# Kernel tuning notes

Measured on AMD Instinct MI355X. Metric: run time of the kernel, lower is better.

Reference implementation:

```python
import jax, jax.numpy as jnp
import numpy as np

INPUT_SIZE = 10000
GROUP_SIZE = 500
STEP = GROUP_SIZE // 2            # 250
OUT_PER_GROUP = 50
GROUPS = 2 * INPUT_SIZE // GROUP_SIZE - 1  # 39


def setup_inputs() -> dict:
    key = jax.random.key(0)
    k1, k2 = jax.random.split(key)
    x = jax.random.uniform(k1, (4096, INPUT_SIZE), dtype=jnp.float32)
    # torch init: uniform_(weight, 0.9, 1.1); weight shape per group is [out, in]
    W = jax.random.uniform(k2, (GROUPS, OUT_PER_GROUP, GROUP_SIZE),
                           dtype=jnp.float32, minval=0.9, maxval=1.1)
    return {"x": x, "W": W}


def reference(x, W):
    # gather overlapping windows: idx[g, k] = g*STEP + k  -> [B, GROUPS, GROUP_SIZE]
    idx = jnp.arange(GROUPS)[:, None] * STEP + jnp.arange(GROUP_SIZE)[None, :]
    xw = x[:, idx]                                   # [B, G, K]
    # per-group linear (no bias): out[b,g,o] = sum_k xw[b,g,k] * W[g,o,k]
    out = jnp.einsum('bgk,gok->bgo', xw, W)          # [B, G, O]
    return jax.nn.relu(out.reshape(x.shape[0], GROUPS * OUT_PER_GROUP))
```

## Files before the change

### kernel.cpp

```cpp
#include <hip/hip_runtime.h>
#include <hip/hip_bf16.h>


constexpr int INPUT  = 10000;
constexpr int GROUPS = 39;
constexpr int GS     = 500;
constexpr int STEP   = 250;
constexpr int OPG    = 50;
constexpr int OUTW   = 1950;
constexpr int KP     = 512;
constexpr int BM     = 32;
constexpr int LDA    = KP + 8;

__device__ __hip_bfloat16 Wb[GROUPS * OPG * KP];

typedef __attribute__((ext_vector_type(8))) short  short8;
typedef __attribute__((ext_vector_type(4))) float  float4v;

__device__ __forceinline__ unsigned bf2pack(float a, float b) {
    union { float f; unsigned u; } x, y; x.f = a; y.f = b;
    unsigned lo = (x.u + 0x7fffu + ((x.u >> 16) & 1u)) >> 16;
    unsigned hi = (y.u + 0x7fffu + ((y.u >> 16) & 1u)) & 0xffff0000u;
    return hi | lo;
}

__global__ void prep_w(const float* __restrict__ W) {
    const int slot = blockIdx.x * 256 + threadIdx.x;
    if (slot >= GROUPS * OPG * (KP / 2)) return;
    const int go = slot / (KP / 2);
    const int k  = (slot - go * (KP / 2)) * 2;
    float2 v = {0.f, 0.f};
    if (k < GS) v = *(const float2*)(W + (size_t)go * GS + k);
    ((unsigned*)Wb)[slot] = bf2pack(v.x, v.y);
}

__global__ __launch_bounds__(256, 4)
void peak_binner_kernel(const float* __restrict__ x,
                        float* __restrict__ out, int batch)
{
    __shared__ __align__(16) short As[BM * LDA];

    const int g    = blockIdx.x;
    const int m0   = blockIdx.y * BM;
    const int tid  = threadIdx.x;
    const int lane = tid & 63;
    const int wave = tid >> 6;
    const int fm   = lane & 15;
    const int l4   = lane >> 4;
    const int nb   = (wave == 3) ? 34 : wave * 16;

    const bool lvalid = (tid < STEP);
    #pragma unroll
    for (int bb = 0; bb < 4; ++bb) {
        float2 v[8];
        #pragma unroll
        for (int j = 0; j < 8; ++j) {
            const int it = bb * 8 + j;
            const int gr = min(m0 + it, batch - 1);
            v[j] = lvalid ? *(const float2*)(x + (size_t)gr * INPUT + g * STEP + 2 * tid)
                          : float2{0.f, 0.f};
        }
        #pragma unroll
        for (int j = 0; j < 8; ++j) {
            const int it = bb * 8 + j;
            *(unsigned*)&As[it * LDA + 2 * tid] = bf2pack(v[j].x, v[j].y);
        }
    }

    float4v acc[2] = {{0,0,0,0},{0,0,0,0}};
    const __hip_bfloat16* wp = Wb + ((size_t)g * OPG + nb + fm) * KP + l4 * 8;

    __syncthreads();

    #pragma unroll
    for (int kk = 0; kk < 16; ++kk) {
        const short8 b  = *(const short8*)(wp + kk * 32);
        const short8 a0 = *(const short8*)&As[fm        * LDA + kk * 32 + l4 * 8];
        const short8 a1 = *(const short8*)&As[(16 + fm) * LDA + kk * 32 + l4 * 8];
        acc[0] = __builtin_amdgcn_mfma_f32_16x16x32_bf16(a0, b, acc[0], 0, 0, 0);
        acc[1] = __builtin_amdgcn_mfma_f32_16x16x32_bf16(a1, b, acc[1], 0, 0, 0);
    }

    if (wave < 3 || fm >= 14) {
        const int col = g * OPG + nb + fm;
        #pragma unroll
        for (int mt = 0; mt < 2; ++mt)
            #pragma unroll
            for (int reg = 0; reg < 4; ++reg) {
                const int row = m0 + mt * 16 + l4 * 4 + reg;
                if (row < batch)
                    out[(size_t)row * OUTW + col] = fmaxf(acc[mt][reg], 0.f);
            }
    }
}

extern "C" void kernel_launch(void* const* d_in, const int* in_sizes, int n_in,
                              void* d_out, int out_size, void* d_ws, size_t ws_size,
                              hipStream_t stream) {
    const float* x = (const float*)d_in[0];
    const float* W = (const float*)d_in[1];
    float* out     = (float*)d_out;

    const int batch = in_sizes[0] / INPUT;

    const int slots = GROUPS * OPG * (KP / 2);
    prep_w<<<(slots + 255) / 256, 256, 0, stream>>>(W);

    dim3 grid(GROUPS, (batch + BM - 1) / BM);
    peak_binner_kernel<<<grid, dim3(256), 0, stream>>>(x, out, batch);
}
```

Measured before the change: 280.7 us.

## Reuse overlapping half-window tiles across consecutive groups with software-pipelined loop

Splits each 500-wide window into two 250-wide halves stored in a 4-slot LDS ring. Each block now walks 9-10 consecutive groups for a 16-row batch tile, so each half of x is converted to bf16 once and reused by two adjacent groups instead of being reloaded. Weights are repacked with padding per half. Global loads for x and W are prefetched one iteration ahead, with manual waitcnt barriers and setprio around the MFMA section. This halves x traffic and conversion work at the cost of a sequential loop per block, fewer blocks, and a batch that must be a multiple of 16 (the row guards are removed).

```diff
diff --git a/kernel.cpp b/kernel.cpp
--- a/kernel.cpp
+++ b/kernel.cpp
@@ -4,18 +4,26 @@
 
 constexpr int INPUT  = 10000;
 constexpr int GROUPS = 39;
-constexpr int GS     = 500;
-constexpr int STEP   = 250;
+constexpr int HALF   = 250;
 constexpr int OPG    = 50;
 constexpr int OUTW   = 1950;
 constexpr int KP     = 512;
-constexpr int BM     = 32;
-constexpr int LDA    = KP + 8;
+constexpr int BMT    = 16;
+constexpr int LDH    = 264;
+constexpr int SLOT   = BMT * LDH;
 
 __device__ __hip_bfloat16 Wb[GROUPS * OPG * KP];
 
-typedef __attribute__((ext_vector_type(8))) short  short8;
-typedef __attribute__((ext_vector_type(4))) float  float4v;
+typedef __attribute__((ext_vector_type(8))) short    short8;
+typedef __attribute__((ext_vector_type(4))) float    float4v;
+typedef __attribute__((ext_vector_type(2))) unsigned uint2v;
+
+#define LGKM_BAR() do { \
+    asm volatile("s_waitcnt lgkmcnt(0)" ::: "memory"); \
+    __builtin_amdgcn_sched_barrier(0); \
+    __builtin_amdgcn_s_barrier(); \
+    __builtin_amdgcn_sched_barrier(0); \
+} while (0)
 
 __device__ __forceinline__ unsigned bf2pack(float a, float b) {
     union { float f; unsigned u; } x, y; x.f = a; y.f = b;
@@ -27,10 +35,11 @@
 __global__ void prep_w(const float* __restrict__ W) {
     const int slot = blockIdx.x * 256 + threadIdx.x;
     if (slot >= GROUPS * OPG * (KP / 2)) return;
-    const int go = slot / (KP / 2);
-    const int k  = (slot - go * (KP / 2)) * 2;
+    const int go = slot >> 8;
+    const int pd = (slot & 255) * 2;
     float2 v = {0.f, 0.f};
-    if (k < GS) v = *(const float2*)(W + (size_t)go * GS + k);
+    if (pd < 250)                      v = *(const float2*)(W + (size_t)go * 500 + pd);
+    else if (pd >= 256 && pd < 506)    v = *(const float2*)(W + (size_t)go * 500 + pd - 6);
     ((unsigned*)Wb)[slot] = bf2pack(v.x, v.y);
 }
 
@@ -38,10 +47,12 @@
 void peak_binner_kernel(const float* __restrict__ x,
                         float* __restrict__ out, int batch)
 {
-    __shared__ __align__(16) short As[BM * LDA];
+    __shared__ __align__(16) short As[4 * SLOT];
 
-    const int g    = blockIdx.x;
-    const int m0   = blockIdx.y * BM;
+    const int my   = blockIdx.x;
+    const int gc   = blockIdx.y;
+    const int g0   = gc * 10;
+    const int NG   = (gc < 3) ? 10 : 9;
     const int tid  = threadIdx.x;
     const int lane = tid & 63;
     const int wave = tid >> 6;
@@ -49,48 +60,84 @@
     const int l4   = lane >> 4;
     const int nb   = (wave == 3) ? 34 : wave * 16;
 
-    const bool lvalid = (tid < STEP);
-    #pragma unroll
-    for (int bb = 0; bb < 4; ++bb) {
-        float2 v[8];
+    const float* xr0 = x + (size_t)(my * BMT + wave * 4) * INPUT + 4 * lane;
+    const __hip_bfloat16* wp = Wb + ((size_t)g0 * OPG + nb + fm) * KP + l4 * 8;
+
+    float4v vS[4];
+    short8  bfrag[16];
+    float4v acc;
+
+    auto LOADB = [&]() {
         #pragma unroll
-        for (int j = 0; j < 8; ++j) {
-            const int it = bb * 8 + j;
-            const int gr = min(m0 + it, batch - 1);
-            v[j] = lvalid ? *(const float2*)(x + (size_t)gr * INPUT + g * STEP + 2 * tid)
-                          : float2{0.f, 0.f};
+        for (int j = 0; j < 16; ++j) bfrag[j] = *(const short8*)(wp + j * 32);
+    };
+
+    auto ISSUE = [&](int h) {
+        const int gh = g0 + h;
+        const float* p0 = xr0 + gh * HALF;
+        if (gh != 39) {
+            #pragma unroll
+            for (int j = 0; j < 4; ++j)
+                vS[j] = *(const float4v*)(p0 + (size_t)j * INPUT);
+        } else {
+            #pragma unroll
+            for (int j = 0; j < 4; ++j) {
+                if (lane < 62)        vS[j] = *(const float4v*)(p0 + (size_t)j * INPUT);
+                else if (lane == 62) { float2 t = *(const float2*)(p0 + (size_t)j * INPUT);
+                                       vS[j] = float4v{t.x, t.y, 0.f, 0.f}; }
+                else                   vS[j] = float4v{0.f, 0.f, 0.f, 0.f};
+            }
+        }
+    };
+
+    auto CONVERT = [&](int s) {
+        #pragma unroll
+        for (int j = 0; j < 4; ++j) {
+            uint2v w;
+            w[0] = bf2pack(vS[j][0], vS[j][1]);
+            w[1] = bf2pack(vS[j][2], vS[j][3]);
+            *(uint2v*)&As[s * SLOT + (wave * 4 + j) * LDH + 4 * lane] = w;
+        }
+    };
+
+    auto COMPUTE = [&](int sA, int sB) {
+        acc = float4v{0.f, 0.f, 0.f, 0.f};
+        const int ab = fm * LDH + l4 * 8;
+        __builtin_amdgcn_s_setprio(1);
+        #pragma unroll
+        for (int kk = 0; kk < 8; ++kk) {
+            const short8 a = *(const short8*)&As[sA * SLOT + ab + kk * 32];
+            acc = __builtin_amdgcn_mfma_f32_16x16x32_bf16(a, bfrag[kk], acc, 0, 0, 0);
         }
         #pragma unroll
-        for (int j = 0; j < 8; ++j) {
-            const int it = bb * 8 + j;
-            *(unsigned*)&As[it * LDA + 2 * tid] = bf2pack(v[j].x, v[j].y);
+        for (int kk = 0; kk < 8; ++kk) {
+            const short8 a = *(const short8*)&As[sB * SLOT + ab + kk * 32];
+            acc = __builtin_amdgcn_mfma_f32_16x16x32_bf16(a, bfrag[8 + kk], acc, 0, 0, 0);
         }
-    }
+        __builtin_amdgcn_s_setprio(0);
+    };
 
-    float4v acc[2] = {{0,0,0,0},{0,0,0,0}};
-    const __hip_bfloat16* wp = Wb + ((size_t)g * OPG + nb + fm) * KP + l4 * 8;
+    auto EPI = [&](int g) {
+        if (wave < 3 || fm >= 14) {
+            const int col = g * OPG + nb + fm;
+            #pragma unroll
+            for (int reg = 0; reg < 4; ++reg)
+                out[(size_t)(my * BMT + l4 * 4 + reg) * OUTW + col] = fmaxf(acc[reg], 0.f);
+        }
+    };
 
-    __syncthreads();
+    ISSUE(0); LOADB(); CONVERT(0);
+    ISSUE(1); CONVERT(1);
+    LGKM_BAR();
 
-    #pragma unroll
-    for (int kk = 0; kk < 16; ++kk) {
-        const short8 b  = *(const short8*)(wp + kk * 32);
-        const short8 a0 = *(const short8*)&As[fm        * LDA + kk * 32 + l4 * 8];
-        const short8 a1 = *(const short8*)&As[(16 + fm) * LDA + kk * 32 + l4 * 8];
-        acc[0] = __builtin_amdgcn_mfma_f32_16x16x32_bf16(a0, b, acc[0], 0, 0, 0);
-        acc[1] = __builtin_amdgcn_mfma_f32_16x16x32_bf16(a1, b, acc[1], 0, 0, 0);
-    }
-
-    if (wave < 3 || fm >= 14) {
-        const int col = g * OPG + nb + fm;
-        #pragma unroll
-        for (int mt = 0; mt < 2; ++mt)
-            #pragma unroll
-            for (int reg = 0; reg < 4; ++reg) {
-                const int row = m0 + mt * 16 + l4 * 4 + reg;
-                if (row < batch)
-                    out[(size_t)row * OUTW + col] = fmaxf(acc[mt][reg], 0.f);
-            }
+    for (int i = 0; i < NG; ++i) {
+        if (i + 2 <= NG) ISSUE(i + 2);
+        COMPUTE(i & 3, (i + 1) & 3);
+        EPI(g0 + i);
+        wp += (size_t)OPG * KP;
+        if (i + 1 < NG) LOADB();
+        if (i + 2 <= NG) CONVERT((i + 2) & 3);
+        LGKM_BAR();
     }
 }
 
@@ -106,6 +153,6 @@
     const int slots = GROUPS * OPG * (KP / 2);
     prep_w<<<(slots + 255) / 256, 256, 0, stream>>>(W);
 
-    dim3 grid(GROUPS, (batch + BM - 1) / BM);
+    dim3 grid(batch / BMT, 4);
     peak_binner_kernel<<<grid, dim3(256), 0, stream>>>(x, out, batch);
 }
```

After: 285.1 us. No clear change (+1.5%).
